# Kernel tuning notes

Hardware: AMD Instinct MI355X
Metric: run time of the kernel (lower is better)

The kernel has to match this reference:

```python
import jax, jax.numpy as jnp
import numpy as np

N_NODES = 50000
N_EDGES = 800000
D = 64
BN_EPS = 1e-5


def setup_inputs() -> dict:
    key = jax.random.key(0)
    ks = jax.random.split(key, 16)
    x = jax.random.normal(ks[0], (N_NODES, D), dtype=jnp.float32)
    edge_index = jax.random.randint(ks[1], (2, N_EDGES), 0, N_NODES, dtype=jnp.int64)
    s = 1.0 / np.sqrt(D)
    def lin(k):
        kw, kb = jax.random.split(k)
        W = jax.random.uniform(kw, (D, D), jnp.float32, -s, s)
        b = jax.random.uniform(kb, (D,), jnp.float32, -s, s)
        return W, b
    W1_0, b1_0 = lin(ks[2])
    W2_0, b2_0 = lin(ks[3])
    W1_1, b1_1 = lin(ks[4])
    W2_1, b2_1 = lin(ks[5])
    return {
        "x": x, "edge_index": edge_index,
        "W1_0": W1_0, "b1_0": b1_0, "g_0": jnp.ones((D,), jnp.float32), "beta_0": jnp.zeros((D,), jnp.float32), "W2_0": W2_0, "b2_0": b2_0,
        "W1_1": W1_1, "b1_1": b1_1, "g_1": jnp.ones((D,), jnp.float32), "beta_1": jnp.zeros((D,), jnp.float32), "W2_1": W2_1, "b2_1": b2_1,
    }


def _gin_layer(x, src, dst, W1, b1, g, beta, W2, b2):
    # GINConv with eps=0: h_i = MLP( x_i + sum_{j->i} x_j )
    agg = jax.ops.segment_sum(x[src], dst, num_segments=N_NODES)  # [N, D]
    h = agg + x
    h = h @ W1 + b1
    # BatchNorm1d (training-mode batch statistics, biased variance)
    mean = jnp.mean(h, axis=0)
    var = jnp.var(h, axis=0)
    h = (h - mean) * jax.lax.rsqrt(var + BN_EPS) * g + beta
    h = jax.nn.relu(h)
    h = jax.nn.relu(h @ W2 + b2)
    return h


def reference(x, edge_index, W1_0, b1_0, g_0, beta_0, W2_0, b2_0,
              W1_1, b1_1, g_1, beta_1, W2_1, b2_1):
    src = edge_index[0]  # message source j
    dst = edge_index[1]  # aggregation target i
    h1 = _gin_layer(x, src, dst, W1_0, b1_0, g_0, beta_0, W2_0, b2_0)
    h2 = _gin_layer(h1, src, dst, W1_1, b1_1, g_1, beta_1, W2_1, b2_1)
    return (h1, h2)
```

## Files before the change

### kernel.cpp

```cpp
#include <hip/hip_runtime.h>
#include <hip/hip_bf16.h>

#define N_NODES 50000
#define N_EDGES 800000
#define DD 64
#define RPB 64
#define GBLOCKS ((N_NODES + RPB - 1) / RPB)
#define MBLOCKS ((N_NODES + 63) / 64)
#define NBUCKET ((N_NODES + 63) / 64)
#define SCAN_BLOCKS ((N_NODES + 255) / 256)
#define CAST_BLOCKS ((N_NODES * DD / 8 + 255) / 256)
#define BN_EPS 1e-5f


__device__ __forceinline__ float bf2f(unsigned short b) {
    return __uint_as_float(((unsigned)b) << 16);
}
__device__ __forceinline__ float loadF(const void* p, int i, int isf) {
    return isf ? ((const float*)p)[i] : bf2f(((const unsigned short*)p)[i]);
}
template<bool ISF>
__device__ __forceinline__ float4 ld4(const void* p, int i) {
    if (ISF) return *reinterpret_cast<const float4*>((const float*)p + i);
    ushort4 u = *reinterpret_cast<const ushort4*>((const unsigned short*)p + i);
    return make_float4(bf2f(u.x), bf2f(u.y), bf2f(u.z), bf2f(u.w));
}
__device__ __forceinline__ void acc8(float4& a, float4& b, uint4 u) {
    a.x += __uint_as_float(u.x << 16);
    a.y += __uint_as_float(u.x & 0xFFFF0000u);
    a.z += __uint_as_float(u.y << 16);
    a.w += __uint_as_float(u.y & 0xFFFF0000u);
    b.x += __uint_as_float(u.z << 16);
    b.y += __uint_as_float(u.z & 0xFFFF0000u);
    b.z += __uint_as_float(u.w << 16);
    b.w += __uint_as_float(u.w & 0xFFFF0000u);
}

__global__ __launch_bounds__(256) void initcast_kernel(
    const void* __restrict__ x, const int* __restrict__ ei,
    int* __restrict__ flags, int* __restrict__ cnt,
    float* __restrict__ sums, unsigned short* __restrict__ xb)
{
    __shared__ int cntF, cntI;
    int t = threadIdx.x;
    if (t == 0) { cntF = 0; cntI = 0; }
    __syncthreads();
    unsigned short wd = ((const unsigned short*)x)[2 * t];
    int e = (wd >> 7) & 0xFF;
    if (e >= 0x70 && e <= 0x8F) atomicAdd(&cntF, 1);
    if (t < 128 && ei[2 * t + 1] == 0) atomicAdd(&cntI, 1);
    __syncthreads();
    int isf = (cntF < 128) ? 1 : 0;

    int gid = blockIdx.x * 256 + t;
    if (gid < N_NODES) cnt[gid] = 0;
    if (gid < 256) sums[gid] = 0.0f;
    if (blockIdx.x == 0 && t == 0) {
        flags[0] = isf;
        flags[1] = (cntI > 64) ? 1 : 0;
    }

    int i = gid * 8;
    if (i < N_NODES * DD) {
        if (isf) {
            float4 a = *reinterpret_cast<const float4*>((const float*)x + i);
            float4 b = *reinterpret_cast<const float4*>((const float*)x + i + 4);
            ushort4 o0, o1;
            o0.x = __bfloat16_as_ushort(__float2bfloat16(a.x));
            o0.y = __bfloat16_as_ushort(__float2bfloat16(a.y));
            o0.z = __bfloat16_as_ushort(__float2bfloat16(a.z));
            o0.w = __bfloat16_as_ushort(__float2bfloat16(a.w));
            o1.x = __bfloat16_as_ushort(__float2bfloat16(b.x));
            o1.y = __bfloat16_as_ushort(__float2bfloat16(b.y));
            o1.z = __bfloat16_as_ushort(__float2bfloat16(b.z));
            o1.w = __bfloat16_as_ushort(__float2bfloat16(b.w));
            *reinterpret_cast<ushort4*>(xb + i) = o0;
            *reinterpret_cast<ushort4*>(xb + i + 4) = o1;
        } else {
            *reinterpret_cast<uint4*>(xb + i) =
                *reinterpret_cast<const uint4*>((const unsigned short*)x + i);
        }
    }
}

__global__ void hist_kernel(const int* __restrict__ ei, int* __restrict__ cnt,
                            const int* __restrict__ flags) {
    int i64 = flags[1];
    int e = blockIdx.x * 256 + threadIdx.x;
    int d = i64 ? ei[2 * N_EDGES + 2 * e] : ei[N_EDGES + e];
    atomicAdd(cnt + d, 1);
}

__global__ __launch_bounds__(256) void scanA_kernel(const int* __restrict__ cnt,
                                                    int* __restrict__ off,
                                                    int* __restrict__ bsum) {
    __shared__ int tmp[256];
    int t = threadIdx.x;
    int i = blockIdx.x * 256 + t;
    int v = (i < N_NODES) ? cnt[i] : 0;
    tmp[t] = v;
    __syncthreads();
    #pragma unroll
    for (int d = 1; d < 256; d <<= 1) {
        int u = (t >= d) ? tmp[t - d] : 0;
        __syncthreads();
        tmp[t] += u;
        __syncthreads();
    }
    if (i < N_NODES) off[i] = tmp[t] - v;
    if (t == 255) bsum[blockIdx.x] = tmp[255];
}

__global__ __launch_bounds__(256) void scanB_kernel(int* __restrict__ bsum,
                                                    int* __restrict__ off) {
    __shared__ int tmp[256];
    int t = threadIdx.x;
    int v = (t < SCAN_BLOCKS) ? bsum[t] : 0;
    tmp[t] = v;
    __syncthreads();
    #pragma unroll
    for (int d = 1; d < 256; d <<= 1) {
        int u = (t >= d) ? tmp[t - d] : 0;
        __syncthreads();
        tmp[t] += u;
        __syncthreads();
    }
    if (t < SCAN_BLOCKS) bsum[t] = tmp[t] - v;
    if (t == 255) off[N_NODES] = tmp[255];
}

__global__ __launch_bounds__(256) void scanC_kernel(const int* __restrict__ bsum,
                                                    int* __restrict__ off,
                                                    int* __restrict__ bcur) {
    int i = blockIdx.x * 256 + threadIdx.x;
    if (i < N_NODES) {
        int o = off[i] + bsum[blockIdx.x];
        off[i] = o;
        if ((i & 63) == 0) bcur[(i >> 6) * 16] = o;
    }
}

__global__ void fillA_kernel(const int* __restrict__ ei, int* __restrict__ bcur,
                             unsigned int* __restrict__ tmp, const int* __restrict__ flags) {
    int i64 = flags[1];
    int e = blockIdx.x * 256 + threadIdx.x;
    int s, d;
    if (i64) { s = ei[2 * e]; d = ei[2 * N_EDGES + 2 * e]; }
    else     { s = ei[e];     d = ei[N_EDGES + e]; }
    int b = d >> 6;
    int pos = atomicAdd(bcur + b * 16, 1);
    tmp[pos] = (unsigned)s | ((unsigned)(d & 63) << 16);
}

__global__ __launch_bounds__(256) void fillB_kernel(const int* __restrict__ off,
                                                    const unsigned int* __restrict__ tmp,
                                                    unsigned short* __restrict__ srt) {
    __shared__ int cur64[64];
    int b = blockIdx.x;
    int t = threadIdx.x;
    if (t < 64) {
        int idx = b * 64 + t;
        cur64[t] = (idx < N_NODES) ? off[idx] : N_EDGES;
    }
    __syncthreads();
    int start = off[b * 64];
    int endn  = (b + 1) * 64; if (endn > N_NODES) endn = N_NODES;
    int end   = off[endn];
    for (int i = start + t; i < end; i += 256) {
        unsigned v = tmp[i];
        int pos = atomicAdd(&cur64[v >> 16], 1);
        srt[pos] = (unsigned short)(v & 0xFFFFu);
    }
}

__global__ __launch_bounds__(512) void gather_gemm_stats_kernel(
    const unsigned short* __restrict__ xb, const void* __restrict__ self_src, int force_f32,
    const int* __restrict__ off, const unsigned short* __restrict__ srt,
    const void* __restrict__ W, const void* __restrict__ bias,
    float* __restrict__ out_, float* __restrict__ sums, const int* __restrict__ flags)
{
    __shared__ float sIn[RPB][DD];
    __shared__ float r1[8][DD], r2[8][DD];
    int tid = threadIdx.x;
    int lane = tid & 63, w = tid >> 6;
    int rs = lane >> 3, ch = lane & 7;
    int row0 = blockIdx.x * RPB;
    int isf = force_f32 ? 1 : flags[0];

    int lr = w * 8 + rs;
    int r = row0 + lr;
    float4 a  = make_float4(0.f, 0.f, 0.f, 0.f);
    float4 b  = make_float4(0.f, 0.f, 0.f, 0.f);
    float4 a2 = make_float4(0.f, 0.f, 0.f, 0.f);
    float4 b2 = make_float4(0.f, 0.f, 0.f, 0.f);
    if (r < N_NODES) {
        a = isf ? ld4<true>(self_src, r * DD + 8 * ch)
                : ld4<false>(self_src, r * DD + 8 * ch);
        b = isf ? ld4<true>(self_src, r * DD + 8 * ch + 4)
                : ld4<false>(self_src, r * DD + 8 * ch + 4);
        int k0 = off[r], k1 = off[r + 1];
        int k = k0;
        for (; k + 8 <= k1; k += 8) {
            int n0 = srt[k],     n1 = srt[k + 1], n2 = srt[k + 2], n3 = srt[k + 3];
            int n4 = srt[k + 4], n5 = srt[k + 5], n6 = srt[k + 6], n7 = srt[k + 7];
            uint4 u0 = *reinterpret_cast<const uint4*>(xb + n0 * DD + 8 * ch);
            uint4 u1 = *reinterpret_cast<const uint4*>(xb + n1 * DD + 8 * ch);
            uint4 u2 = *reinterpret_cast<const uint4*>(xb + n2 * DD + 8 * ch);
            uint4 u3 = *reinterpret_cast<const uint4*>(xb + n3 * DD + 8 * ch);
            uint4 u4 = *reinterpret_cast<const uint4*>(xb + n4 * DD + 8 * ch);
            uint4 u5 = *reinterpret_cast<const uint4*>(xb + n5 * DD + 8 * ch);
            uint4 u6 = *reinterpret_cast<const uint4*>(xb + n6 * DD + 8 * ch);
            uint4 u7 = *reinterpret_cast<const uint4*>(xb + n7 * DD + 8 * ch);
            acc8(a, b, u0);
            acc8(a2, b2, u1);
            acc8(a, b, u2);
            acc8(a2, b2, u3);
            acc8(a, b, u4);
            acc8(a2, b2, u5);
            acc8(a, b, u6);
            acc8(a2, b2, u7);
        }
        for (; k + 2 <= k1; k += 2) {
            int n0 = srt[k], n1 = srt[k + 1];
            uint4 u0 = *reinterpret_cast<const uint4*>(xb + n0 * DD + 8 * ch);
            uint4 u1 = *reinterpret_cast<const uint4*>(xb + n1 * DD + 8 * ch);
            acc8(a, b, u0);
            acc8(a2, b2, u1);
        }
        if (k < k1) {
            int n0 = srt[k];
            acc8(a, b, *reinterpret_cast<const uint4*>(xb + n0 * DD + 8 * ch));
        }
        a.x += a2.x; a.y += a2.y; a.z += a2.z; a.w += a2.w;
        b.x += b2.x; b.y += b2.y; b.z += b2.z; b.w += b2.w;
    }
    *reinterpret_cast<float4*>(&sIn[lr][8 * ch]) = a;
    *reinterpret_cast<float4*>(&sIn[lr][8 * ch + 4]) = b;
    __syncthreads();

    float wcol[DD];
    #pragma unroll
    for (int k = 0; k < DD; ++k) wcol[k] = loadF(W, k * DD + lane, isf);
    float bv = loadF(bias, lane, isf);

    float s1 = 0.f, s2 = 0.f;
    #pragma unroll 4
    for (int j = 0; j < 8; ++j) {
        int jr = w * 8 + j;
        float c0 = 0.f, c1 = 0.f, c2 = 0.f, c3 = 0.f;
        #pragma unroll
        for (int k = 0; k < DD; k += 4) {
            float4 aa = *reinterpret_cast<const float4*>(&sIn[jr][k]);
            c0 += aa.x * wcol[k];
            c1 += aa.y * wcol[k + 1];
            c2 += aa.z * wcol[k + 2];
            c3 += aa.w * wcol[k + 3];
        }
        float acc = bv + ((c0 + c1) + (c2 + c3));
        int rr = row0 + jr;
        if (rr < N_NODES) {
            out_[rr * DD + lane] = acc;
            s1 += acc;
            s2 += acc * acc;
        }
    }
    r1[w][lane] = s1; r2[w][lane] = s2;
    __syncthreads();
    if (w == 0) {
        float t1 = 0.f, t2 = 0.f;
        #pragma unroll
        for (int q = 0; q < 8; ++q) { t1 += r1[q][lane]; t2 += r2[q][lane]; }
        atomicAdd(&sums[lane], t1);
        atomicAdd(&sums[64 + lane], t2);
    }
}

__global__ __launch_bounds__(256) void mlp2_kernel(
    const float* __restrict__ in_, const float* __restrict__ sums,
    const void* __restrict__ gma, const void* __restrict__ beta,
    const void* __restrict__ W, const void* __restrict__ bias,
    float* __restrict__ oF, unsigned short* obf, const int* __restrict__ flags)
{
    __shared__ float sIn[64][DD];
    __shared__ float sScale[DD], sShift[DD];
    int isf = flags[0];
    int tid = threadIdx.x;
    int c = tid & 63, g = tid >> 6;
    int row0 = blockIdx.x * 64;

    if (tid < 64) {
        float S1 = sums[tid];
        float S2 = sums[64 + tid];
        float mean = S1 * (1.0f / N_NODES);
        float var  = S2 * (1.0f / N_NODES) - mean * mean;
        float scale = rsqrtf(var + BN_EPS) * loadF(gma, tid, isf);
        sScale[tid] = scale;
        sShift[tid] = loadF(beta, tid, isf) - mean * scale;
    }
    __syncthreads();

    #pragma unroll
    for (int j = 0; j < 4; ++j) {
        int lr = (tid >> 4) + 16 * j;
        int cc = (tid & 15) << 2;
        int r = row0 + lr;
        float4 v = make_float4(0.f, 0.f, 0.f, 0.f);
        if (r < N_NODES) {
            v = *reinterpret_cast<const float4*>(in_ + r * DD + cc);
            float4 sc = *reinterpret_cast<const float4*>(&sScale[cc]);
            float4 sh = *reinterpret_cast<const float4*>(&sShift[cc]);
            v.x = fmaxf(v.x * sc.x + sh.x, 0.f);
            v.y = fmaxf(v.y * sc.y + sh.y, 0.f);
            v.z = fmaxf(v.z * sc.z + sh.z, 0.f);
            v.w = fmaxf(v.w * sc.w + sh.w, 0.f);
        }
        *reinterpret_cast<float4*>(&sIn[lr][cc]) = v;
    }
    __syncthreads();

    float wcol[DD];
    #pragma unroll
    for (int k = 0; k < DD; ++k) wcol[k] = loadF(W, k * DD + c, isf);
    float bv = loadF(bias, c, isf);

    #pragma unroll 4
    for (int j = 0; j < 16; ++j) {
        int lr = g * 16 + j;
        float a0 = 0.f, a1 = 0.f, a2 = 0.f, a3 = 0.f;
        #pragma unroll
        for (int k = 0; k < DD; k += 4) {
            float4 a = *reinterpret_cast<const float4*>(&sIn[lr][k]);
            a0 += a.x * wcol[k];
            a1 += a.y * wcol[k + 1];
            a2 += a.z * wcol[k + 2];
            a3 += a.w * wcol[k + 3];
        }
        float acc = fmaxf(bv + ((a0 + a1) + (a2 + a3)), 0.f);
        int r = row0 + lr;
        if (r < N_NODES) {
            oF[r * DD + c] = acc;
            if (obf) obf[r * DD + c] = __bfloat16_as_ushort(__float2bfloat16(acc));
        }
    }
}

extern "C" void kernel_launch(void* const* d_in, const int* in_sizes, int n_in,
                              void* d_out, int out_size, void* d_ws, size_t ws_size,
                              hipStream_t stream)
{
    (void)in_sizes; (void)n_in; (void)out_size; (void)ws_size;
    const void* x  = d_in[0];
    const int* ei  = (const int*)d_in[1];
    const void* W1_0 = d_in[2];  const void* b1_0 = d_in[3];
    const void* g_0  = d_in[4];  const void* be_0 = d_in[5];
    const void* W2_0 = d_in[6];  const void* b2_0 = d_in[7];
    const void* W1_1 = d_in[8];  const void* b1_1 = d_in[9];
    const void* g_1  = d_in[10]; const void* be_1 = d_in[11];
    const void* W2_1 = d_in[12]; const void* b2_1 = d_in[13];

    float* wsf   = (float*)d_ws;
    float* sumsA = wsf;
    float* sumsB = wsf + 128;
    int*  flags  = (int*)(wsf + 256);
    int*  cnt    = (int*)(wsf + 512);
    int*  off    = cnt + 50048;
    int*  bcur   = off + 50064;
    int*  bsum   = bcur + 12512;
    unsigned int* tmp32 = (unsigned int*)(bsum + 256) + 48;
    unsigned short* srt = (unsigned short*)(tmp32 + 800000);
    unsigned short* xb  = srt + 800064;
    float* O1    = (float*)d_out;
    float* O2    = O1 + (size_t)N_NODES * DD;

    dim3 blk(256);

    initcast_kernel<<<CAST_BLOCKS, blk, 0, stream>>>(x, ei, flags, cnt, sumsA, xb);
    hist_kernel<<<N_EDGES / 256, blk, 0, stream>>>(ei, cnt, flags);
    scanA_kernel<<<SCAN_BLOCKS, blk, 0, stream>>>(cnt, off, bsum);
    scanB_kernel<<<1, blk, 0, stream>>>(bsum, off);
    scanC_kernel<<<SCAN_BLOCKS, blk, 0, stream>>>(bsum, off, bcur);
    fillA_kernel<<<N_EDGES / 256, blk, 0, stream>>>(ei, bcur, tmp32, flags);
    fillB_kernel<<<NBUCKET, blk, 0, stream>>>(off, tmp32, srt);

    gather_gemm_stats_kernel<<<GBLOCKS, 512, 0, stream>>>(xb, x, 0, off, srt, W1_0, b1_0,
                                                          O2, sumsA, flags);
    mlp2_kernel<<<MBLOCKS, blk, 0, stream>>>(O2, sumsA, g_0, be_0, W2_0, b2_0, O1, xb, flags);

    gather_gemm_stats_kernel<<<GBLOCKS, 512, 0, stream>>>(xb, O1, 1, off, srt, W1_1, b1_1,
                                                          O2, sumsB, flags);
    mlp2_kernel<<<MBLOCKS, blk, 0, stream>>>(O2, sumsB, g_1, be_1, W2_1, b2_1, O2, nullptr, flags);
}
```

Before: 306.7 us.

## Split neighbor gather across two half-groups and fuse scan block-sum pass

The gather kernel now processes 32 rows per block. Each row's edge list is split between two groups of four waves, and the partial sums go to padded shared arrays that are added together inside the GEMM loop. This doubles the parallelism per row and shortens serial gather chains, at the cost of more blocks, redundant weight loads per block, and extra shared-memory reads. Separately, the single-block scanB pass is folded into scanC: every block rescans the block sums locally, which removes one kernel launch.

```diff
diff --git a/kernel.cpp b/kernel.cpp
--- a/kernel.cpp
+++ b/kernel.cpp
@@ -4,7 +4,8 @@
 #define N_NODES 50000
 #define N_EDGES 800000
 #define DD 64
-#define RPB 64
+#define RPB 32
+#define PADD 68
 #define GBLOCKS ((N_NODES + RPB - 1) / RPB)
 #define MBLOCKS ((N_NODES + 63) / 64)
 #define NBUCKET ((N_NODES + 63) / 64)
@@ -111,8 +112,9 @@
     if (t == 255) bsum[blockIdx.x] = tmp[255];
 }
 
-__global__ __launch_bounds__(256) void scanB_kernel(int* __restrict__ bsum,
-                                                    int* __restrict__ off) {
+__global__ __launch_bounds__(256) void scanC_kernel(const int* __restrict__ bsum,
+                                                    int* __restrict__ off,
+                                                    int* __restrict__ bcur) {
     __shared__ int tmp[256];
     int t = threadIdx.x;
     int v = (t < SCAN_BLOCKS) ? bsum[t] : 0;
@@ -125,19 +127,14 @@
         tmp[t] += u;
         __syncthreads();
     }
-    if (t < SCAN_BLOCKS) bsum[t] = tmp[t] - v;
-    if (t == 255) off[N_NODES] = tmp[255];
-}
-
-__global__ __launch_bounds__(256) void scanC_kernel(const int* __restrict__ bsum,
-                                                    int* __restrict__ off,
-                                                    int* __restrict__ bcur) {
-    int i = blockIdx.x * 256 + threadIdx.x;
+    int base = (blockIdx.x == 0) ? 0 : tmp[blockIdx.x - 1];
+    int i = blockIdx.x * 256 + t;
     if (i < N_NODES) {
-        int o = off[i] + bsum[blockIdx.x];
+        int o = off[i] + base;
         off[i] = o;
         if ((i & 63) == 0) bcur[(i >> 6) * 16] = o;
     }
+    if (blockIdx.x == SCAN_BLOCKS - 1 && t == 0) off[N_NODES] = tmp[SCAN_BLOCKS - 1];
 }
 
 __global__ void fillA_kernel(const int* __restrict__ ei, int* __restrict__ bcur,
@@ -179,28 +176,34 @@
     const void* __restrict__ W, const void* __restrict__ bias,
     float* __restrict__ out_, float* __restrict__ sums, const int* __restrict__ flags)
 {
-    __shared__ float sIn[RPB][DD];
+    __shared__ float sPart[2][RPB][PADD];
     __shared__ float r1[8][DD], r2[8][DD];
     int tid = threadIdx.x;
     int lane = tid & 63, w = tid >> 6;
+    int half = w >> 2;
+    int wg = w & 3;
     int rs = lane >> 3, ch = lane & 7;
     int row0 = blockIdx.x * RPB;
     int isf = force_f32 ? 1 : flags[0];
 
-    int lr = w * 8 + rs;
+    int lr = wg * 8 + rs;
     int r = row0 + lr;
     float4 a  = make_float4(0.f, 0.f, 0.f, 0.f);
     float4 b  = make_float4(0.f, 0.f, 0.f, 0.f);
     float4 a2 = make_float4(0.f, 0.f, 0.f, 0.f);
     float4 b2 = make_float4(0.f, 0.f, 0.f, 0.f);
     if (r < N_NODES) {
-        a = isf ? ld4<true>(self_src, r * DD + 8 * ch)
-                : ld4<false>(self_src, r * DD + 8 * ch);
-        b = isf ? ld4<true>(self_src, r * DD + 8 * ch + 4)
-                : ld4<false>(self_src, r * DD + 8 * ch + 4);
+        if (half == 0) {
+            a = isf ? ld4<true>(self_src, r * DD + 8 * ch)
+                    : ld4<false>(self_src, r * DD + 8 * ch);
+            b = isf ? ld4<true>(self_src, r * DD + 8 * ch + 4)
+                    : ld4<false>(self_src, r * DD + 8 * ch + 4);
+        }
         int k0 = off[r], k1 = off[r + 1];
-        int k = k0;
-        for (; k + 8 <= k1; k += 8) {
+        int mid = k0 + ((k1 - k0 + 1) >> 1);
+        int k  = half ? mid : k0;
+        int ke = half ? k1 : mid;
+        for (; k + 8 <= ke; k += 8) {
             int n0 = srt[k],     n1 = srt[k + 1], n2 = srt[k + 2], n3 = srt[k + 3];
             int n4 = srt[k + 4], n5 = srt[k + 5], n6 = srt[k + 6], n7 = srt[k + 7];
             uint4 u0 = *reinterpret_cast<const uint4*>(xb + n0 * DD + 8 * ch);
@@ -220,22 +223,22 @@
             acc8(a, b, u6);
             acc8(a2, b2, u7);
         }
-        for (; k + 2 <= k1; k += 2) {
+        for (; k + 2 <= ke; k += 2) {
             int n0 = srt[k], n1 = srt[k + 1];
             uint4 u0 = *reinterpret_cast<const uint4*>(xb + n0 * DD + 8 * ch);
             uint4 u1 = *reinterpret_cast<const uint4*>(xb + n1 * DD + 8 * ch);
             acc8(a, b, u0);
             acc8(a2, b2, u1);
         }
-        if (k < k1) {
+        if (k < ke) {
             int n0 = srt[k];
             acc8(a, b, *reinterpret_cast<const uint4*>(xb + n0 * DD + 8 * ch));
         }
         a.x += a2.x; a.y += a2.y; a.z += a2.z; a.w += a2.w;
         b.x += b2.x; b.y += b2.y; b.z += b2.z; b.w += b2.w;
     }
-    *reinterpret_cast<float4*>(&sIn[lr][8 * ch]) = a;
-    *reinterpret_cast<float4*>(&sIn[lr][8 * ch + 4]) = b;
+    *reinterpret_cast<float4*>(&sPart[half][lr][8 * ch]) = a;
+    *reinterpret_cast<float4*>(&sPart[half][lr][8 * ch + 4]) = b;
     __syncthreads();
 
     float wcol[DD];
@@ -244,17 +247,18 @@
     float bv = loadF(bias, lane, isf);
 
     float s1 = 0.f, s2 = 0.f;
-    #pragma unroll 4
-    for (int j = 0; j < 8; ++j) {
-        int jr = w * 8 + j;
+    #pragma unroll
+    for (int j = 0; j < 4; ++j) {
+        int jr = w * 4 + j;
         float c0 = 0.f, c1 = 0.f, c2 = 0.f, c3 = 0.f;
         #pragma unroll
         for (int k = 0; k < DD; k += 4) {
-            float4 aa = *reinterpret_cast<const float4*>(&sIn[jr][k]);
-            c0 += aa.x * wcol[k];
-            c1 += aa.y * wcol[k + 1];
-            c2 += aa.z * wcol[k + 2];
-            c3 += aa.w * wcol[k + 3];
+            float4 p0 = *reinterpret_cast<const float4*>(&sPart[0][jr][k]);
+            float4 p1 = *reinterpret_cast<const float4*>(&sPart[1][jr][k]);
+            c0 += (p0.x + p1.x) * wcol[k];
+            c1 += (p0.y + p1.y) * wcol[k + 1];
+            c2 += (p0.z + p1.z) * wcol[k + 2];
+            c3 += (p0.w + p1.w) * wcol[k + 3];
         }
         float acc = bv + ((c0 + c1) + (c2 + c3));
         int rr = row0 + jr;
@@ -377,7 +381,6 @@
     initcast_kernel<<<CAST_BLOCKS, blk, 0, stream>>>(x, ei, flags, cnt, sumsA, xb);
     hist_kernel<<<N_EDGES / 256, blk, 0, stream>>>(ei, cnt, flags);
     scanA_kernel<<<SCAN_BLOCKS, blk, 0, stream>>>(cnt, off, bsum);
-    scanB_kernel<<<1, blk, 0, stream>>>(bsum, off);
     scanC_kernel<<<SCAN_BLOCKS, blk, 0, stream>>>(bsum, off, bcur);
     fillA_kernel<<<N_EDGES / 256, blk, 0, stream>>>(ei, bcur, tmp32, flags);
     fillB_kernel<<<NBUCKET, blk, 0, stream>>>(off, tmp32, srt);
```

New measurement: 372.3 us. 1.21x slower.
